# Kernel tuning notes

Hardware: AMD Instinct MI355X
Metric: run time of the kernel (lower is better)

The kernel has to match this reference:

```python
import jax, jax.numpy as jnp
import numpy as np

NUM_HEADING_BIN = 12
NUM_SIZE_CLUSTER = 8
DELTA_NORM_W = 0.01
CENTER_W = 0.5
B, N = 4096, 2048


def huber(err, delta=1.0):
    a = jnp.abs(err)
    q = jnp.minimum(a, delta)
    return jnp.mean(0.5 * q * q + delta * (a - q))


def box3d_corners(centers, headings, sizes):
    # centers (B,3), headings (B,), sizes (B,3) -> (B,8,3)
    l, w, h = sizes[:, 0:1], sizes[:, 1:2], sizes[:, 2:3]
    sx = jnp.asarray([1, 1, -1, -1, 1, 1, -1, -1], dtype=sizes.dtype)
    sy = jnp.asarray([1, -1, -1, 1, 1, -1, -1, 1], dtype=sizes.dtype)
    sz = jnp.asarray([1, 1, 1, 1, -1, -1, -1, -1], dtype=sizes.dtype)
    corners = jnp.stack([0.5 * l * sx, 0.5 * w * sy, 0.5 * h * sz], axis=1)  # (B,3,8)
    c, s = jnp.cos(headings), jnp.sin(headings)
    z, o = jnp.zeros_like(c), jnp.ones_like(c)
    R = jnp.stack([jnp.stack([c, -s, z], -1),
                   jnp.stack([s, c, z], -1),
                   jnp.stack([z, z, o], -1)], axis=1)  # (B,3,3)
    out = jnp.einsum('bij,bjk->bik', R, corners) + centers[:, :, None]
    return jnp.transpose(out, (0, 2, 1))  # (B,8,3)


def setup_inputs() -> dict:
    key = jax.random.key(0)
    ks = jax.random.split(key, 9)
    return {
        'mask_xyz_mean': jax.random.normal(ks[0], (B, 3), jnp.float32),
        'point_cloud': jax.random.normal(ks[1], (B, 3, N), jnp.float32),
        'x_delta': jax.random.normal(ks[2], (B, 3, N), jnp.float32),
        'center_label': jax.random.normal(ks[3], (B, 3), jnp.float32),
        'size_residual_label': jax.random.normal(ks[4], (B, 3), jnp.float32),
        'heading_residual_label': jax.random.normal(ks[5], (B,), jnp.float32),
        'mean_sizes': jax.random.uniform(ks[6], (NUM_SIZE_CLUSTER, 3), jnp.float32, 0.5, 2.5),
        'size_class_label': jax.random.randint(ks[7], (B,), 0, NUM_SIZE_CLUSTER, jnp.int32),
        'heading_class_label': jax.random.randint(ks[8], (B,), 0, NUM_HEADING_BIN, jnp.int32),
    }


def reference(mask_xyz_mean, point_cloud, x_delta, center_label,
              size_residual_label, heading_residual_label, mean_sizes,
              size_class_label, heading_class_label):
    eps = 0.0  # faithful: original has no eps
    # center loss
    center_dist = jnp.linalg.norm(mask_xyz_mean - center_label, axis=1)
    center_loss = CENTER_W * huber(center_dist)

    # label assembly (onehot-sum == gather)
    size_label = mean_sizes[size_class_label] + size_residual_label  # (B,3)
    bin_centers = jnp.arange(0, np.pi, np.pi / NUM_HEADING_BIN, dtype=jnp.float32)
    heading_label = heading_residual_label + bin_centers[heading_class_label]  # (B,)

    corners_3d_gt = box3d_corners(center_label, heading_label, size_label)
    corners_2d_gt = corners_3d_gt[:, 4:8, :2]  # (B,4,2)

    v = center_label[:, :2]  # (B,2)
    p_dir = jnp.stack([-v[:, 1], v[:, 0]], axis=1)
    p_dir = p_dir / jnp.linalg.norm(p_dir, axis=1, keepdims=True)  # (B,2)

    pp_label = jnp.einsum('bkc,bc->bk', corners_2d_gt, p_dir)  # (B,4)
    py_max, py_min = jnp.max(pp_label, axis=1), jnp.min(pp_label, axis=1)
    std_y_label = (py_max - py_min) / 4
    mean_y_label = (py_max + py_min) / 2

    v_norm = jnp.linalg.norm(v, axis=1, keepdims=True)  # (B,1)
    proj_label = jnp.einsum('bkc,bc->bk', corners_2d_gt, v) / v_norm  # (B,4)
    p_max, p_min = jnp.max(proj_label, axis=1), jnp.min(proj_label, axis=1)
    std_label = (p_max - p_min) / 4
    mean_label = (p_max + p_min) / 2

    pc_xy = jnp.transpose(point_cloud, (0, 2, 1))[:, :, :2]  # (B,N,2)

    pp_pc = jnp.einsum('bnc,bc->bn', pc_xy, p_dir)  # (B,N)
    std_y_pc = jnp.std(pp_pc, axis=1, ddof=1)
    mean_y_pc = jnp.mean(pp_pc, axis=1)
    y_std_loss = huber(jnp.abs(std_y_label - std_y_pc))
    y_mean_loss = huber(jnp.abs(mean_y_label - mean_y_pc))

    proj_pc = jnp.einsum('bnc,bc->bn', pc_xy, v) / v_norm  # (B,N)
    std_pc = jnp.std(proj_pc, axis=1, ddof=1)
    mean_pc = jnp.mean(proj_pc, axis=1)
    x_std_loss = huber(jnp.abs(std_label - std_pc))
    x_mean_loss = huber(jnp.abs(mean_label - mean_pc))

    delta_norm = jnp.sqrt(jnp.sum(x_delta * x_delta, axis=(1, 2)))
    delta_norm_loss = DELTA_NORM_W * huber(delta_norm)

    total = center_loss + x_std_loss + x_mean_loss + delta_norm_loss + y_mean_loss + y_std_loss
    return 0.4 * total
```

## Files before the change

kernel.cpp:

```cpp
#include <hip/hip_runtime.h>
#include <math.h>

#define B_SZ 4096
#define N_PTS 2048
#define BLOCK 256

__device__ __forceinline__ float huber1(float a) {
    float q = fminf(a, 1.0f);
    return 0.5f * q * q + (a - q);
}

__global__ __launch_bounds__(BLOCK) void loss_stage1(
    const float* __restrict__ point_cloud,
    const float* __restrict__ x_delta,
    const float* __restrict__ center_label,
    float4* __restrict__ ws_pc,
    float*  __restrict__ ws_d)
{
    const int b    = blockIdx.x >> 1;
    const int role = blockIdx.x & 1;
    const int tid  = threadIdx.x;
    const int wave = tid >> 6;
    const int lane = tid & 63;

    const size_t base = (size_t)b * 3 * N_PTS;

    __shared__ float red[BLOCK / 64][4];

    if (role == 0) {
        const float cx = center_label[b * 3 + 0];
        const float cy = center_label[b * 3 + 1];
        const float vnorm  = sqrtf(cx * cx + cy * cy);
        const float pdx = -cy / vnorm;
        const float pdy =  cx / vnorm;

        const float4* px4 = (const float4*)(point_cloud + base);
        const float4* py4 = (const float4*)(point_cloud + base + N_PTS);

        const float4 x0 = px4[tid];
        const float4 x1 = px4[tid + BLOCK];
        const float4 y0 = py4[tid];
        const float4 y1 = py4[tid + BLOCK];

        float s_pp = 0.f, s_pp2 = 0.f, s_t = 0.f, s_t2 = 0.f;
        const float xs[8] = {x0.x, x0.y, x0.z, x0.w, x1.x, x1.y, x1.z, x1.w};
        const float ys[8] = {y0.x, y0.y, y0.z, y0.w, y1.x, y1.y, y1.z, y1.w};
        #pragma unroll
        for (int j = 0; j < 8; ++j) {
            const float pp = xs[j] * pdx + ys[j] * pdy;
            const float t  = xs[j] * cx  + ys[j] * cy;
            s_pp += pp; s_pp2 += pp * pp; s_t += t; s_t2 += t * t;
        }

        #pragma unroll
        for (int off = 32; off > 0; off >>= 1) {
            s_pp  += __shfl_down(s_pp,  off, 64);
            s_pp2 += __shfl_down(s_pp2, off, 64);
            s_t   += __shfl_down(s_t,   off, 64);
            s_t2  += __shfl_down(s_t2,  off, 64);
        }
        if (lane == 0) {
            red[wave][0] = s_pp;  red[wave][1] = s_pp2;
            red[wave][2] = s_t;   red[wave][3] = s_t2;
        }
        __syncthreads();
        if (tid == 0) {
            #pragma unroll
            for (int w = 1; w < BLOCK / 64; ++w) {
                s_pp  += red[w][0];
                s_pp2 += red[w][1];
                s_t   += red[w][2];
                s_t2  += red[w][3];
            }
            ws_pc[b] = make_float4(s_pp, s_pp2, s_t, s_t2);
        }
    } else {
        const float4* pd4 = (const float4*)(x_delta + base);

        float4 d[6];
        #pragma unroll
        for (int k = 0; k < 6; ++k) d[k] = pd4[tid + k * BLOCK];

        float a0 = 0.f, a1 = 0.f, a2 = 0.f, a3 = 0.f;
        #pragma unroll
        for (int k = 0; k < 6; ++k) {
            a0 += d[k].x * d[k].x;
            a1 += d[k].y * d[k].y;
            a2 += d[k].z * d[k].z;
            a3 += d[k].w * d[k].w;
        }
        float s_d2 = (a0 + a1) + (a2 + a3);

        #pragma unroll
        for (int off = 32; off > 0; off >>= 1)
            s_d2 += __shfl_down(s_d2, off, 64);

        if (lane == 0) red[wave][0] = s_d2;
        __syncthreads();
        if (tid == 0) {
            #pragma unroll
            for (int w = 1; w < BLOCK / 64; ++w) s_d2 += red[w][0];
            ws_d[b] = s_d2;
        }
    }
}

__global__ __launch_bounds__(BLOCK) void loss_stage2(
    const float4* __restrict__ ws_pc,
    const float*  __restrict__ ws_d,
    const float* __restrict__ mask_xyz_mean,
    const float* __restrict__ center_label,
    const float* __restrict__ size_residual,
    const float* __restrict__ heading_residual,
    const float* __restrict__ mean_sizes,
    const int*   __restrict__ size_class,
    const int*   __restrict__ heading_class,
    float* __restrict__ ws_p)
{
    const int tid = threadIdx.x;
    const int b   = blockIdx.x * BLOCK + tid;

    const float4 pcs = ws_pc[b];
    const float s_pp = pcs.x, s_pp2 = pcs.y, s_t = pcs.z, s_t2 = pcs.w;
    const float s_d2 = ws_d[b];

    const float cx = center_label[b * 3 + 0];
    const float cy = center_label[b * 3 + 1];
    const float cz = center_label[b * 3 + 2];
    const float vnorm2 = cx * cx + cy * cy;
    const float vnorm  = sqrtf(vnorm2);
    const float pdx = -cy / vnorm;
    const float pdy =  cx / vnorm;

    const float mx = mask_xyz_mean[b * 3 + 0];
    const float my = mask_xyz_mean[b * 3 + 1];
    const float mz = mask_xyz_mean[b * 3 + 2];
    const float dxc = mx - cx, dyc = my - cy, dzc = mz - cz;
    const float center_dist = sqrtf(dxc * dxc + dyc * dyc + dzc * dzc);

    const int sc = size_class[b];
    const float l  = mean_sizes[sc * 3 + 0] + size_residual[b * 3 + 0];
    const float w_ = mean_sizes[sc * 3 + 1] + size_residual[b * 3 + 1];

    const float theta = heading_residual[b] +
                        (float)heading_class[b] * (float)(M_PI / 12.0);
    const float c = cosf(theta);
    const float s = sinf(theta);
    const float hl = 0.5f * l, hw = 0.5f * w_;

    float X[4], Y[4];
    X[0] =  c * hl - s * hw + cx;  Y[0] =  s * hl + c * hw + cy;
    X[1] =  c * hl + s * hw + cx;  Y[1] =  s * hl - c * hw + cy;
    X[2] = -c * hl + s * hw + cx;  Y[2] = -s * hl - c * hw + cy;
    X[3] = -c * hl - s * hw + cx;  Y[3] = -s * hl + c * hw + cy;

    float ppmax = -INFINITY, ppmin = INFINITY;
    float pmax  = -INFINITY, pmin  = INFINITY;
    #pragma unroll
    for (int k = 0; k < 4; ++k) {
        const float pp = X[k] * pdx + Y[k] * pdy;
        const float pj = (X[k] * cx + Y[k] * cy) / vnorm;
        ppmax = fmaxf(ppmax, pp); ppmin = fminf(ppmin, pp);
        pmax  = fmaxf(pmax,  pj); pmin  = fminf(pmin,  pj);
    }
    const float std_y_label  = (ppmax - ppmin) * 0.25f;
    const float mean_y_label = (ppmax + ppmin) * 0.5f;
    const float std_label    = (pmax - pmin) * 0.25f;
    const float mean_label   = (pmax + pmin) * 0.5f;

    const float invN   = 1.0f / (float)N_PTS;
    const float invNm1 = 1.0f / (float)(N_PTS - 1);

    const float mean_y_pc = s_pp * invN;
    const float var_y = (s_pp2 - s_pp * s_pp * invN) * invNm1;
    const float std_y_pc = sqrtf(fmaxf(var_y, 0.0f));

    const float mean_pc = (s_t * invN) / vnorm;
    const float var_x = ((s_t2 - s_t * s_t * invN) * invNm1) / vnorm2;
    const float std_pc = sqrtf(fmaxf(var_x, 0.0f));

    const float delta_norm = sqrtf(s_d2);

    float total =
          0.5f  * huber1(center_dist)
        +         huber1(fabsf(std_label  - std_pc))
        +         huber1(fabsf(mean_label - mean_pc))
        + 0.01f * huber1(delta_norm)
        +         huber1(fabsf(mean_y_label - mean_y_pc))
        +         huber1(fabsf(std_y_label  - std_y_pc));

    #pragma unroll
    for (int off = 32; off > 0; off >>= 1)
        total += __shfl_down(total, off, 64);

    __shared__ float red[BLOCK / 64];
    const int wave = tid >> 6;
    const int lane = tid & 63;
    if (lane == 0) red[wave] = total;
    __syncthreads();
    if (tid == 0) {
        #pragma unroll
        for (int w = 1; w < BLOCK / 64; ++w) total += red[w];
        ws_p[blockIdx.x] = total;
    }
}

__global__ void loss_stage3(const float* __restrict__ ws_p, float* __restrict__ out)
{
    const int lane = threadIdx.x;
    float s = (lane < B_SZ / BLOCK) ? ws_p[lane] : 0.0f;
    #pragma unroll
    for (int off = 32; off > 0; off >>= 1)
        s += __shfl_down(s, off, 64);
    if (lane == 0) out[0] = s * (0.4f / (float)B_SZ);
}

extern "C" void kernel_launch(void* const* d_in, const int* in_sizes, int n_in,
                              void* d_out, int out_size, void* d_ws, size_t ws_size,
                              hipStream_t stream) {
    const float* mask_xyz_mean    = (const float*)d_in[0];
    const float* point_cloud      = (const float*)d_in[1];
    const float* x_delta          = (const float*)d_in[2];
    const float* center_label     = (const float*)d_in[3];
    const float* size_residual    = (const float*)d_in[4];
    const float* heading_residual = (const float*)d_in[5];
    const float* mean_sizes       = (const float*)d_in[6];
    const int*   size_class       = (const int*)d_in[7];
    const int*   heading_class    = (const int*)d_in[8];
    float* out = (float*)d_out;

    float4* ws_pc = (float4*)d_ws;
    float*  ws_d  = (float*)d_ws + B_SZ * 4;
    float*  ws_p  = ws_d + B_SZ;

    loss_stage1<<<2 * B_SZ, BLOCK, 0, stream>>>(
        point_cloud, x_delta, center_label, ws_pc, ws_d);
    loss_stage2<<<B_SZ / BLOCK, BLOCK, 0, stream>>>(
        ws_pc, ws_d, mask_xyz_mean, center_label, size_residual,
        heading_residual, mean_sizes, size_class, heading_class, ws_p);
    loss_stage3<<<1, 64, 0, stream>>>(ws_p, out);
}
```

Baseline: 222.1 us.

## Assign each batch row to a 16-lane group instead of a whole block

Stage 1 now launches 512 blocks instead of 8192. Each 16-lane subgroup of a wave handles one batch row and loops over all of that row's points, so shared-memory reductions and __syncthreads are replaced by 16-lane shuffles. The aim is to cut per-block launch and synchronisation overhead and keep more loads in flight per thread. The risk is fewer waves in flight: only 2048 waves across the GPU, each with long serial loops, which may not hide memory latency on a bandwidth-bound kernel. Each 16-lane group reads 256 contiguous bytes per load.

```diff
diff --git a/kernel.cpp b/kernel.cpp
--- a/kernel.cpp
+++ b/kernel.cpp
@@ -17,91 +17,82 @@
     float4* __restrict__ ws_pc,
     float*  __restrict__ ws_d)
 {
-    const int b    = blockIdx.x >> 1;
-    const int role = blockIdx.x & 1;
     const int tid  = threadIdx.x;
     const int wave = tid >> 6;
     const int lane = tid & 63;
-
-    const size_t base = (size_t)b * 3 * N_PTS;
-
-    __shared__ float red[BLOCK / 64][4];
-
-    if (role == 0) {
-        const float cx = center_label[b * 3 + 0];
-        const float cy = center_label[b * 3 + 1];
-        const float vnorm  = sqrtf(cx * cx + cy * cy);
-        const float pdx = -cy / vnorm;
-        const float pdy =  cx / vnorm;
-
-        const float4* px4 = (const float4*)(point_cloud + base);
-        const float4* py4 = (const float4*)(point_cloud + base + N_PTS);
-
-        const float4 x0 = px4[tid];
-        const float4 x1 = px4[tid + BLOCK];
-        const float4 y0 = py4[tid];
-        const float4 y1 = py4[tid + BLOCK];
+    const int g    = lane >> 4;
+    const int il   = lane & 15;
+
+    if (blockIdx.x < 256) {
+        const int quad = blockIdx.x * 4 + wave;
+        const int e    = quad * 4 + g;
+
+        const float cx = center_label[e * 3 + 0];
+        const float cy = center_label[e * 3 + 1];
+        const float vn = sqrtf(cx * cx + cy * cy);
+        const float pdx = -cy / vn;
+        const float pdy =  cx / vn;
+
+        const float4* px = (const float4*)(point_cloud + (size_t)e * 3 * N_PTS);
+        const float4* py = px + (N_PTS / 4);
 
         float s_pp = 0.f, s_pp2 = 0.f, s_t = 0.f, s_t2 = 0.f;
-        const float xs[8] = {x0.x, x0.y, x0.z, x0.w, x1.x, x1.y, x1.z, x1.w};
-        const float ys[8] = {y0.x, y0.y, y0.z, y0.w, y1.x, y1.y, y1.z, y1.w};
+
+        #pragma unroll 4
+        for (int k = 0; k < N_PTS / 4 / 16; ++k) {
+            const float4 x4 = px[il + k * 16];
+            const float4 y4 = py[il + k * 16];
+            {
+                const float pp = x4.x * pdx + y4.x * pdy;
+                const float t  = x4.x * cx  + y4.x * cy;
+                s_pp += pp; s_pp2 += pp * pp; s_t += t; s_t2 += t * t;
+            }
+            {
+                const float pp = x4.y * pdx + y4.y * pdy;
+                const float t  = x4.y * cx  + y4.y * cy;
+                s_pp += pp; s_pp2 += pp * pp; s_t += t; s_t2 += t * t;
+            }
+            {
+                const float pp = x4.z * pdx + y4.z * pdy;
+                const float t  = x4.z * cx  + y4.z * cy;
+                s_pp += pp; s_pp2 += pp * pp; s_t += t; s_t2 += t * t;
+            }
+            {
+                const float pp = x4.w * pdx + y4.w * pdy;
+                const float t  = x4.w * cx  + y4.w * cy;
+                s_pp += pp; s_pp2 += pp * pp; s_t += t; s_t2 += t * t;
+            }
+        }
+
         #pragma unroll
-        for (int j = 0; j < 8; ++j) {
-            const float pp = xs[j] * pdx + ys[j] * pdy;
-            const float t  = xs[j] * cx  + ys[j] * cy;
-            s_pp += pp; s_pp2 += pp * pp; s_t += t; s_t2 += t * t;
-        }
-
-        #pragma unroll
-        for (int off = 32; off > 0; off >>= 1) {
+        for (int off = 8; off > 0; off >>= 1) {
             s_pp  += __shfl_down(s_pp,  off, 64);
             s_pp2 += __shfl_down(s_pp2, off, 64);
             s_t   += __shfl_down(s_t,   off, 64);
             s_t2  += __shfl_down(s_t2,  off, 64);
         }
-        if (lane == 0) {
-            red[wave][0] = s_pp;  red[wave][1] = s_pp2;
-            red[wave][2] = s_t;   red[wave][3] = s_t2;
+        if (il == 0) ws_pc[e] = make_float4(s_pp, s_pp2, s_t, s_t2);
+    } else {
+        const int quad = (blockIdx.x - 256) * 4 + wave;
+        const int e    = quad * 4 + g;
+
+        const float4* pd = (const float4*)(x_delta + (size_t)e * 3 * N_PTS);
+
+        float a0 = 0.f, a1 = 0.f, a2 = 0.f, a3 = 0.f;
+        #pragma unroll 8
+        for (int k = 0; k < 3 * N_PTS / 4 / 16; ++k) {
+            const float4 d = pd[il + k * 16];
+            a0 += d.x * d.x;
+            a1 += d.y * d.y;
+            a2 += d.z * d.z;
+            a3 += d.w * d.w;
         }
-        __syncthreads();
-        if (tid == 0) {
-            #pragma unroll
-            for (int w = 1; w < BLOCK / 64; ++w) {
-                s_pp  += red[w][0];
-                s_pp2 += red[w][1];
-                s_t   += red[w][2];
-                s_t2  += red[w][3];
-            }
-            ws_pc[b] = make_float4(s_pp, s_pp2, s_t, s_t2);
-        }
-    } else {
-        const float4* pd4 = (const float4*)(x_delta + base);
-
-        float4 d[6];
+        float s = (a0 + a1) + (a2 + a3);
+
         #pragma unroll
-        for (int k = 0; k < 6; ++k) d[k] = pd4[tid + k * BLOCK];
-
-        float a0 = 0.f, a1 = 0.f, a2 = 0.f, a3 = 0.f;
-        #pragma unroll
-        for (int k = 0; k < 6; ++k) {
-            a0 += d[k].x * d[k].x;
-            a1 += d[k].y * d[k].y;
-            a2 += d[k].z * d[k].z;
-            a3 += d[k].w * d[k].w;
-        }
-        float s_d2 = (a0 + a1) + (a2 + a3);
-
-        #pragma unroll
-        for (int off = 32; off > 0; off >>= 1)
-            s_d2 += __shfl_down(s_d2, off, 64);
-
-        if (lane == 0) red[wave][0] = s_d2;
-        __syncthreads();
-        if (tid == 0) {
-            #pragma unroll
-            for (int w = 1; w < BLOCK / 64; ++w) s_d2 += red[w][0];
-            ws_d[b] = s_d2;
-        }
+        for (int off = 8; off > 0; off >>= 1)
+            s += __shfl_down(s, off, 64);
+        if (il == 0) ws_d[e] = s;
     }
 }
 
@@ -233,7 +224,7 @@
     float*  ws_d  = (float*)d_ws + B_SZ * 4;
     float*  ws_p  = ws_d + B_SZ;
 
-    loss_stage1<<<2 * B_SZ, BLOCK, 0, stream>>>(
+    loss_stage1<<<512, BLOCK, 0, stream>>>(
         point_cloud, x_delta, center_label, ws_pc, ws_d);
     loss_stage2<<<B_SZ / BLOCK, BLOCK, 0, stream>>>(
         ws_pc, ws_d, mask_xyz_mean, center_label, size_residual,
```

Measured after the change: 227.7 us. 2.5% more time.
